# Kernel tuning notes

Measured on AMD Instinct MI355X. Metric: run time of the kernel, lower is better.

Reference implementation:

```python
import jax, jax.numpy as jnp
import numpy as np

SAMPLING_RATE = 0.5

def setup_inputs() -> dict:
    key = jax.random.key(0)
    k1, k2 = jax.random.split(key)
    token = jax.random.normal(k1, (8, 16, 4, 384), dtype=jnp.float32)
    feature = jax.random.normal(k2, (8, 16, 4, 196, 384), dtype=jnp.float32)
    return {"token": token, "feature": feature}

def reference(token, feature):
    b1, n1, kk1, c = token.shape
    b2, n2, kk2, hw, _ = feature.shape
    N = n1 * kk1  # == n2 * kk2
    tok = token.reshape(b1, N, 1, c)           # [b, N, 1, c]
    feat = feature.reshape(b2, N, hw, c)       # [b, N, hw, c]
    scale = c ** (-0.5)
    # attention scores: [b, N, 1, hw]
    attn = jnp.einsum('bnqc,bnhc->bnqh', tok, feat) * scale
    attn = jax.nn.softmax(attn, axis=-1)
    tk = int(hw * SAMPLING_RATE)
    sel_attn, sel_idx = jax.lax.top_k(attn, tk)          # [b, N, 1, tk]
    sel_attn = sel_attn / jnp.sum(sel_attn, axis=-1, keepdims=True)
    # gather selected features: idx [b, N, tk] -> feat rows [b, N, tk, c]
    idx = sel_idx[:, :, 0, :]                            # [b, N, tk]
    sel_feat = jnp.take_along_axis(feat, idx[..., None], axis=2)  # [b, N, tk, c]
    out = jnp.einsum('bnqt,bntc->bnqc', sel_attn, sel_feat)       # [b, N, 1, c]
    return out.reshape(b1, n1, kk1, c)
```

## Files before the change

### kernel.cpp

```cpp
#include <hip/hip_runtime.h>
#include <hip/hip_fp16.h>

#define HW 196
#define C  384
#define CF4 (C/4)
#define TK 98
#define NT 512
#define NWAVE (NT/64)

__global__ __launch_bounds__(NT, 2) void sampling_kernel(
    const float* __restrict__ token,
    const float* __restrict__ feature,
    float* __restrict__ out)
{
    __shared__ __align__(16) unsigned char stash_raw[HW * C * 2];
    __shared__ float tokLds[C];
    __shared__ float score[HW];
    __shared__ float selW[TK];
    __shared__ int   selIdx[TK];
    __shared__ int   rank2[2 * HW];
    __shared__ float wsum[NWAVE];
    __shared__ float s_max, s_winv;

    __half (*feat16)[C] = (__half(*)[C])stash_raw;
    float  (*part)[C]   = (float(*)[C])stash_raw;

    const int tid  = threadIdx.x;
    const int wave = tid >> 6;
    const int lane = tid & 63;
    const int l8   = lane & 7;
    const int g8   = lane >> 3;
    const int pair = blockIdx.x;

    const float* tokp = token + (size_t)pair * C;
    const float4* f4base = (const float4*)(feature + (size_t)pair * (HW * C));
    const float4* t4 = (const float4*)tokLds;

    for (int i = tid; i < C; i += NT) tokLds[i] = tokp[i];
    __syncthreads();

    float4 tok[12];
    #pragma unroll
    for (int k = 0; k < 12; ++k) tok[k] = t4[l8 + 8 * k];

    const float scale = 0.05103103630798288f;

    #pragma unroll
    for (int it = 0; it < 3; ++it) {
        const int r = it * 64 + wave * 8 + g8;
        const float4* fr = f4base + (size_t)r * CF4 + l8;
        float4 a[12];
        #pragma unroll
        for (int k = 0; k < 12; ++k) a[k] = fr[8 * k];
        float4 acc = make_float4(0.f, 0.f, 0.f, 0.f);
        #pragma unroll
        for (int k = 0; k < 12; ++k) {
            acc.x += a[k].x * tok[k].x; acc.y += a[k].y * tok[k].y;
            acc.z += a[k].z * tok[k].z; acc.w += a[k].w * tok[k].w;
            union { uint2 u; __half2 h[2]; } W;
            W.h[0] = __floats2half2_rn(a[k].x, a[k].y);
            W.h[1] = __floats2half2_rn(a[k].z, a[k].w);
            *(uint2*)&feat16[r][4 * l8 + 32 * k] = W.u;
        }
        float s = (acc.x + acc.y) + (acc.z + acc.w);
        s += __shfl_xor(s, 1, 64);
        s += __shfl_xor(s, 2, 64);
        s += __shfl_xor(s, 4, 64);
        if (l8 == 0) score[r] = s * scale;
    }
    if (wave < 4 && g8 == 0) {
        const int r = 192 + wave;
        const float4* fr = f4base + (size_t)r * CF4 + l8;
        float4 acc = make_float4(0.f, 0.f, 0.f, 0.f);
        #pragma unroll
        for (int k = 0; k < 12; ++k) {
            float4 a = fr[8 * k];
            acc.x += a.x * tok[k].x; acc.y += a.y * tok[k].y;
            acc.z += a.z * tok[k].z; acc.w += a.w * tok[k].w;
            union { uint2 u; __half2 h[2]; } W;
            W.h[0] = __floats2half2_rn(a.x, a.y);
            W.h[1] = __floats2half2_rn(a.z, a.w);
            *(uint2*)&feat16[r][4 * l8 + 32 * k] = W.u;
        }
        float s = (acc.x + acc.y) + (acc.z + acc.w);
        s += __shfl_xor(s, 1, 64);
        s += __shfl_xor(s, 2, 64);
        s += __shfl_xor(s, 4, 64);
        if (l8 == 0) score[r] = s * scale;
    }
    __syncthreads();

    if (tid < 2 * HW) {
        const int i = tid >> 1, h = tid & 1;
        const float si = score[i];
        int cnt = 0;
        const int j0 = h * (HW / 2);
        for (int j = j0; j < j0 + HW / 2; ++j) {
            const float sj = score[j];
            cnt += (int)((sj > si) | ((sj == si) & (j < i)));
        }
        rank2[tid] = cnt;
    } else if (wave == NWAVE - 1) {
        float m = -3.4e38f;
        for (int i = lane; i < HW; i += 64) m = fmaxf(m, score[i]);
        #pragma unroll
        for (int off = 32; off > 0; off >>= 1)
            m = fmaxf(m, __shfl_xor(m, off, 64));
        if (lane == 0) s_max = m;
    }
    __syncthreads();

    float w = 0.f;
    if (tid < HW) {
        const int rank = rank2[2 * tid] + rank2[2 * tid + 1];
        if (rank < TK) {
            w = __expf(score[tid] - s_max);
            selIdx[rank] = tid;
            selW[rank]  = w;
        }
    }
    #pragma unroll
    for (int off = 32; off > 0; off >>= 1) w += __shfl_xor(w, off, 64);
    if (lane == 0) wsum[wave] = w;
    __syncthreads();
    if (tid == 0) {
        float s = 0.f;
        #pragma unroll
        for (int i = 0; i < NWAVE; ++i) s += wsum[i];
        s_winv = 1.f / s;
    }
    __syncthreads();

    float4 acc_a = make_float4(0.f, 0.f, 0.f, 0.f);
    float4 acc_b = make_float4(0.f, 0.f, 0.f, 0.f);
    #pragma unroll
    for (int j = 0; j < 13; ++j) {
        const int i = wave + NWAVE * j;
        if (i < TK) {
            const int   r   = selIdx[i];
            const float wgt = selW[i];
            union { uint2 u; __half2 h[2]; } U;
            U.u = *(const uint2*)&feat16[r][4 * lane];
            float2 f0 = __half22float2(U.h[0]);
            float2 f1 = __half22float2(U.h[1]);
            acc_a.x += wgt * f0.x; acc_a.y += wgt * f0.y;
            acc_a.z += wgt * f1.x; acc_a.w += wgt * f1.y;
            if (lane < 32) {
                union { uint2 u; __half2 h[2]; } V;
                V.u = *(const uint2*)&feat16[r][256 + 4 * lane];
                float2 g0 = __half22float2(V.h[0]);
                float2 g1 = __half22float2(V.h[1]);
                acc_b.x += wgt * g0.x; acc_b.y += wgt * g0.y;
                acc_b.z += wgt * g1.x; acc_b.w += wgt * g1.y;
            }
        }
    }
    __syncthreads();

    float4* pw = (float4*)&part[wave][0];
    pw[lane] = acc_a;
    if (lane < 32) pw[64 + lane] = acc_b;
    __syncthreads();

    if (tid < C) {
        float s = 0.f;
        #pragma unroll
        for (int wv = 0; wv < NWAVE; ++wv) s += part[wv][tid];
        out[(size_t)pair * C + tid] = s * s_winv;
    }
}

extern "C" void kernel_launch(void* const* d_in, const int* in_sizes, int n_in,
                              void* d_out, int out_size, void* d_ws, size_t ws_size,
                              hipStream_t stream) {
    const float* token   = (const float*)d_in[0];
    const float* feature = (const float*)d_in[1];
    float* out = (float*)d_out;
    const int pairs = in_sizes[0] / C;
    sampling_kernel<<<pairs, NT, 0, stream>>>(token, feature, out);
}
```

Before: 39.47 us.

## Halve LDS stash and re-read upper selected rows from global memory

Only the first TK feature rows are stashed in LDS as fp16. This halves shared memory use so launch bounds can ask for 4 blocks per CU instead of 2. Selected rows are split into a low group, read from the LDS stash, and a high group, re-fetched from global memory (likely L2-resident) four rows at a time in fp32. The cost is extra global reads and a serial O(TK) partition step per thread, traded for higher occupancy and less LDS write traffic.

```diff
diff --git a/kernel.cpp b/kernel.cpp
--- a/kernel.cpp
+++ b/kernel.cpp
@@ -8,22 +8,29 @@
 #define NT 512
 #define NWAVE (NT/64)
 
-__global__ __launch_bounds__(NT, 2) void sampling_kernel(
+__global__ __launch_bounds__(NT, 4) void sampling_kernel(
     const float* __restrict__ token,
     const float* __restrict__ feature,
     float* __restrict__ out)
 {
-    __shared__ __align__(16) unsigned char stash_raw[HW * C * 2];
+    __shared__ __align__(16) unsigned char stash_raw[TK * C * 2];
     __shared__ float tokLds[C];
     __shared__ float score[HW];
     __shared__ float selW[TK];
     __shared__ int   selIdx[TK];
-    __shared__ int   rank2[2 * HW];
     __shared__ float wsum[NWAVE];
+    __shared__ int   uni[2 * HW];
+    __shared__ int   cntG;
     __shared__ float s_max, s_winv;
 
     __half (*feat16)[C] = (__half(*)[C])stash_raw;
     float  (*part)[C]   = (float(*)[C])stash_raw;
+
+    int*   rank2 = uni;
+    int*   lIdx  = uni;
+    int*   gIdx  = uni + TK;
+    float* lW    = (float*)(uni + 2 * TK);
+    float* gW    = (float*)(uni + 3 * TK);
 
     const int tid  = threadIdx.x;
     const int wave = tid >> 6;
@@ -57,10 +64,15 @@
         for (int k = 0; k < 12; ++k) {
             acc.x += a[k].x * tok[k].x; acc.y += a[k].y * tok[k].y;
             acc.z += a[k].z * tok[k].z; acc.w += a[k].w * tok[k].w;
-            union { uint2 u; __half2 h[2]; } W;
-            W.h[0] = __floats2half2_rn(a[k].x, a[k].y);
-            W.h[1] = __floats2half2_rn(a[k].z, a[k].w);
-            *(uint2*)&feat16[r][4 * l8 + 32 * k] = W.u;
+        }
+        if (r < TK) {
+            #pragma unroll
+            for (int k = 0; k < 12; ++k) {
+                union { uint2 u; __half2 h[2]; } W;
+                W.h[0] = __floats2half2_rn(a[k].x, a[k].y);
+                W.h[1] = __floats2half2_rn(a[k].z, a[k].w);
+                *(uint2*)&feat16[r][4 * l8 + 32 * k] = W.u;
+            }
         }
         float s = (acc.x + acc.y) + (acc.z + acc.w);
         s += __shfl_xor(s, 1, 64);
@@ -77,10 +89,6 @@
             float4 a = fr[8 * k];
             acc.x += a.x * tok[k].x; acc.y += a.y * tok[k].y;
             acc.z += a.z * tok[k].z; acc.w += a.w * tok[k].w;
-            union { uint2 u; __half2 h[2]; } W;
-            W.h[0] = __floats2half2_rn(a.x, a.y);
-            W.h[1] = __floats2half2_rn(a.z, a.w);
-            *(uint2*)&feat16[r][4 * l8 + 32 * k] = W.u;
         }
         float s = (acc.x + acc.y) + (acc.z + acc.w);
         s += __shfl_xor(s, 1, 64);
@@ -123,7 +131,20 @@
     for (int off = 32; off > 0; off >>= 1) w += __shfl_xor(w, off, 64);
     if (lane == 0) wsum[wave] = w;
     __syncthreads();
-    if (tid == 0) {
+
+    if (tid < TK) {
+        const int  r   = selIdx[tid];
+        const bool isG = (r >= TK);
+        int pos = 0, cg = 0;
+        for (int j = 0; j < TK; ++j) {
+            const bool g = (selIdx[j] >= TK);
+            cg  += (int)g;
+            pos += (int)((j < tid) & (g == isG));
+        }
+        if (isG) { gIdx[pos] = r; gW[pos] = selW[tid]; }
+        else     { lIdx[pos] = r; lW[pos] = selW[tid]; }
+        if (tid == 0) cntG = cg;
+    } else if (tid == NT - 1) {
         float s = 0.f;
         #pragma unroll
         for (int i = 0; i < NWAVE; ++i) s += wsum[i];
@@ -133,26 +154,68 @@
 
     float4 acc_a = make_float4(0.f, 0.f, 0.f, 0.f);
     float4 acc_b = make_float4(0.f, 0.f, 0.f, 0.f);
-    #pragma unroll
-    for (int j = 0; j < 13; ++j) {
-        const int i = wave + NWAVE * j;
-        if (i < TK) {
-            const int   r   = selIdx[i];
-            const float wgt = selW[i];
-            union { uint2 u; __half2 h[2]; } U;
-            U.u = *(const uint2*)&feat16[r][4 * lane];
-            float2 f0 = __half22float2(U.h[0]);
-            float2 f1 = __half22float2(U.h[1]);
-            acc_a.x += wgt * f0.x; acc_a.y += wgt * f0.y;
-            acc_a.z += wgt * f1.x; acc_a.w += wgt * f1.y;
+    const int cg = cntG;
+    for (int base = wave * 4; base < cg; base += 4 * NWAVE) {
+        const int n = min(4, cg - base);
+        if (n == 4) {
+            const int r0 = gIdx[base + 0], r1 = gIdx[base + 1];
+            const int r2 = gIdx[base + 2], r3 = gIdx[base + 3];
+            const float w0 = gW[base + 0], w1 = gW[base + 1];
+            const float w2 = gW[base + 2], w3 = gW[base + 3];
+            const float4* p0 = f4base + (size_t)r0 * CF4;
+            const float4* p1 = f4base + (size_t)r1 * CF4;
+            const float4* p2 = f4base + (size_t)r2 * CF4;
+            const float4* p3 = f4base + (size_t)r3 * CF4;
+            float4 A0 = p0[lane], A1 = p1[lane], A2 = p2[lane], A3 = p3[lane];
+            float4 B0, B1, B2, B3;
             if (lane < 32) {
-                union { uint2 u; __half2 h[2]; } V;
-                V.u = *(const uint2*)&feat16[r][256 + 4 * lane];
-                float2 g0 = __half22float2(V.h[0]);
-                float2 g1 = __half22float2(V.h[1]);
-                acc_b.x += wgt * g0.x; acc_b.y += wgt * g0.y;
-                acc_b.z += wgt * g1.x; acc_b.w += wgt * g1.y;
-            }
+                B0 = p0[64 + lane]; B1 = p1[64 + lane];
+                B2 = p2[64 + lane]; B3 = p3[64 + lane];
+            }
+            acc_a.x += w0*A0.x + w1*A1.x + w2*A2.x + w3*A3.x;
+            acc_a.y += w0*A0.y + w1*A1.y + w2*A2.y + w3*A3.y;
+            acc_a.z += w0*A0.z + w1*A1.z + w2*A2.z + w3*A3.z;
+            acc_a.w += w0*A0.w + w1*A1.w + w2*A2.w + w3*A3.w;
+            if (lane < 32) {
+                acc_b.x += w0*B0.x + w1*B1.x + w2*B2.x + w3*B3.x;
+                acc_b.y += w0*B0.y + w1*B1.y + w2*B2.y + w3*B3.y;
+                acc_b.z += w0*B0.z + w1*B1.z + w2*B2.z + w3*B3.z;
+                acc_b.w += w0*B0.w + w1*B1.w + w2*B2.w + w3*B3.w;
+            }
+        } else {
+            for (int k = 0; k < n; ++k) {
+                const int   r   = gIdx[base + k];
+                const float wgt = gW[base + k];
+                const float4* p = f4base + (size_t)r * CF4;
+                float4 A = p[lane];
+                acc_a.x += wgt*A.x; acc_a.y += wgt*A.y;
+                acc_a.z += wgt*A.z; acc_a.w += wgt*A.w;
+                if (lane < 32) {
+                    float4 B = p[64 + lane];
+                    acc_b.x += wgt*B.x; acc_b.y += wgt*B.y;
+                    acc_b.z += wgt*B.z; acc_b.w += wgt*B.w;
+                }
+            }
+        }
+    }
+
+    const int cl = TK - cg;
+    for (int j = wave; j < cl; j += NWAVE) {
+        const int   r   = lIdx[j];
+        const float wgt = lW[j];
+        union { uint2 u; __half2 h[2]; } U;
+        U.u = *(const uint2*)&feat16[r][4 * lane];
+        float2 f0 = __half22float2(U.h[0]);
+        float2 f1 = __half22float2(U.h[1]);
+        acc_a.x += wgt * f0.x; acc_a.y += wgt * f0.y;
+        acc_a.z += wgt * f1.x; acc_a.w += wgt * f1.y;
+        if (lane < 32) {
+            union { uint2 u; __half2 h[2]; } V;
+            V.u = *(const uint2*)&feat16[r][256 + 4 * lane];
+            float2 g0 = __half22float2(V.h[0]);
+            float2 g1 = __half22float2(V.h[1]);
+            acc_b.x += wgt * g0.x; acc_b.y += wgt * g0.y;
+            acc_b.z += wgt * g1.x; acc_b.w += wgt * g1.y;
         }
     }
     __syncthreads();
```

After: 39.51 us. About the same (+0.1%).
